# Kernel optimization log

Measured on AMD Instinct MI355X. Metric: run time of the kernel, lower is better.

The kernel has to match this reference:

```python
import jax, jax.numpy as jnp
import numpy as np

CAPACITY_FACTOR = 1.0


def setup_inputs() -> dict:
    key = jax.random.key(0)
    k1, k2, k3, k4 = jax.random.split(key, 4)
    B, T, D, E, F = 4, 2048, 2048, 8, 8192
    hidden_states = jax.random.normal(k1, (B, T, D), dtype=jnp.float32)
    w_gate = jax.random.normal(k2, (D, E), dtype=jnp.float32) * 0.02
    w1 = jax.random.normal(k3, (E, D, F), dtype=jnp.float32) * 0.02
    w2 = jax.random.normal(k4, (E, F, D), dtype=jnp.float32) * 0.02
    return {"hidden_states": hidden_states, "w_gate": w_gate, "w1": w1, "w2": w2}


def _top1_gate(x, w_gate):
    # x: [S, D]; deepspeed top1gating (no noise, no rts, drop_tokens=True)
    S, E = x.shape[0], w_gate.shape[1]
    capacity = int(CAPACITY_FACTOR * S / E)
    logits = x @ w_gate                      # [S, E]
    gates = jax.nn.softmax(logits, axis=-1)  # [S, E]
    idx1 = jnp.argmax(gates, axis=-1)        # [S]
    mask1 = jax.nn.one_hot(idx1, E, dtype=gates.dtype)          # [S, E]
    locations1 = jnp.cumsum(mask1, axis=0) - mask1              # position within expert
    mask1 = mask1 * (locations1 < capacity)                     # drop over-capacity tokens
    locations1_s = jnp.sum(locations1 * mask1, axis=1).astype(jnp.int32)  # [S]
    gates_masked = gates * mask1                                # [S, E]
    loc_oh = jax.nn.one_hot(locations1_s, capacity, dtype=gates.dtype) * jnp.sum(mask1, axis=1, keepdims=True)
    combine_weights = jnp.einsum('se,sc->sec', gates_masked, loc_oh)      # [S, E, C]
    dispatch_mask = (combine_weights > 0).astype(gates.dtype)             # [S, E, C]
    return combine_weights, dispatch_mask


def reference(hidden_states, w_gate, w1, w2):
    B, T, D = hidden_states.shape
    x = hidden_states.reshape(-1, D)                     # [S, D]
    combine_weights, dispatch_mask = _top1_gate(x, w_gate)
    # dense dispatch: [S,E,C] x [S,D] -> [E,C,D]
    dispatched = jnp.einsum('sec,sm->ecm', dispatch_mask, x)
    # per-expert FFN (GELU MLP), batched over experts
    h = jax.nn.gelu(jnp.einsum('ecd,edf->ecf', dispatched, w1))
    expert_out = jnp.einsum('ecf,efd->ecd', h, w2)       # [E, C, D]
    # dense combine: [S,E,C] x [E,C,D] -> [S,D]
    combined = jnp.einsum('sec,ecm->sm', combine_weights, expert_out)
    return combined.reshape(B, T, D)
```

## Files before the change

### kernel.cpp

```cpp
#include <hip/hip_runtime.h>

using u16 = unsigned short;
typedef __attribute__((ext_vector_type(4))) float f32x4;
typedef __attribute__((ext_vector_type(8))) short bf16x8;
typedef unsigned short u16x8 __attribute__((ext_vector_type(8)));

static constexpr int S_TOK = 8192;
static constexpr int NE    = 8;
static constexpr int CAP   = 1024;
static constexpr int DDIM  = 2048;
static constexpr int FDIM  = 8192;

#define S_WAIT_ALL() asm volatile("s_waitcnt vmcnt(0) lgkmcnt(0)" ::: "memory")
#define S_BAR()                                  \
  do {                                           \
    __builtin_amdgcn_sched_barrier(0);           \
    __builtin_amdgcn_s_barrier();                \
    __builtin_amdgcn_sched_barrier(0);           \
  } while (0)

__device__ __forceinline__ u16 f2bf(float f) {
  union { float fv; unsigned uv; } v; v.fv = f;
  unsigned r = v.uv + 0x7fffu + ((v.uv >> 16) & 1u);
  return (u16)(r >> 16);
}

__device__ __forceinline__ float gelu_tanh(float x) {
  float u = 0.7978845608028654f * (x + 0.044715f * x * x * x);
  float t = 1.0f - 2.0f / (__expf(2.0f * u) + 1.0f);
  return 0.5f * x * (1.0f + t);
}

__device__ __forceinline__ void gl_lds16(const void* g, void* l) {
  __builtin_amdgcn_global_load_lds(
      (const __attribute__((address_space(1))) unsigned int*)g,
      (__attribute__((address_space(3))) unsigned int*)l, 16, 0, 0);
}

__global__ __launch_bounds__(256) void fill_zero_kernel(float4* __restrict__ p, int n4) {
  int i = blockIdx.x * 256 + threadIdx.x;
  int stride = gridDim.x * 256;
  float4 z = {0.f, 0.f, 0.f, 0.f};
  for (; i < n4; i += stride) p[i] = z;
}

__global__ __launch_bounds__(256) void gating_kernel(
    const float* __restrict__ x, const float* __restrict__ wg,
    int* __restrict__ tok_expert, float* __restrict__ tok_gate) {
  int s = blockIdx.x * 4 + (threadIdx.x >> 6);
  int lane = threadIdx.x & 63;
  const float4* xv = (const float4*)(x + (size_t)s * DDIM + lane * 32);
  float acc[8];
#pragma unroll
  for (int e = 0; e < 8; ++e) acc[e] = 0.f;
#pragma unroll
  for (int j = 0; j < 8; ++j) {
    float4 xx = xv[j];
#pragma unroll
    for (int c = 0; c < 4; ++c) {
      int i = lane * 32 + j * 4 + c;
      const float4* wrow = (const float4*)(wg + (size_t)i * 8);
      float4 w0 = wrow[0], w1 = wrow[1];
      float xe = (c == 0) ? xx.x : (c == 1) ? xx.y : (c == 2) ? xx.z : xx.w;
      acc[0] += xe * w0.x; acc[1] += xe * w0.y; acc[2] += xe * w0.z; acc[3] += xe * w0.w;
      acc[4] += xe * w1.x; acc[5] += xe * w1.y; acc[6] += xe * w1.z; acc[7] += xe * w1.w;
    }
  }
#pragma unroll
  for (int off = 32; off > 0; off >>= 1)
#pragma unroll
    for (int e = 0; e < 8; ++e) acc[e] += __shfl_xor(acc[e], off, 64);
  if (lane == 0) {
    float m = acc[0]; int ai = 0;
#pragma unroll
    for (int e = 1; e < 8; ++e) if (acc[e] > m) { m = acc[e]; ai = e; }
    float sum = 0.f;
#pragma unroll
    for (int e = 0; e < 8; ++e) sum += expf(acc[e] - m);
    tok_expert[s] = ai;
    tok_gate[s] = 1.0f / sum;
  }
}

__global__ void init_slots(int* tok_of_slot, float* gate_of_slot) {
  int i = blockIdx.x * 256 + threadIdx.x;
  tok_of_slot[i] = -1;
  gate_of_slot[i] = 0.f;
}

__global__ __launch_bounds__(1024) void scan_kernel(
    const int* __restrict__ tok_expert, const float* __restrict__ tok_gate,
    int* __restrict__ tok_of_slot, float* __restrict__ gate_of_slot) {
  __shared__ int cnt[1024][8];
  int t = threadIdx.x;
  int e8[8];
  int local[8];
#pragma unroll
  for (int e = 0; e < 8; ++e) local[e] = 0;
#pragma unroll
  for (int j = 0; j < 8; ++j) {
    int e = tok_expert[t * 8 + j];
    e8[j] = e;
    local[e]++;
  }
#pragma unroll
  for (int e = 0; e < 8; ++e) cnt[t][e] = local[e];
  __syncthreads();
  for (int off = 1; off < 1024; off <<= 1) {
    int v[8];
    bool has = (t >= off);
    if (has) {
#pragma unroll
      for (int e = 0; e < 8; ++e) v[e] = cnt[t - off][e];
    }
    __syncthreads();
    if (has) {
#pragma unroll
      for (int e = 0; e < 8; ++e) cnt[t][e] += v[e];
    }
    __syncthreads();
  }
  int base[8];
#pragma unroll
  for (int e = 0; e < 8; ++e) base[e] = (t == 0) ? 0 : cnt[t - 1][e];
#pragma unroll
  for (int j = 0; j < 8; ++j) {
    int s = t * 8 + j;
    int e = e8[j];
    int p = base[e]++;
    if (p < CAP) {
      tok_of_slot[e * CAP + p] = s;
      gate_of_slot[e * CAP + p] = tok_gate[s];
    }
  }
}

__global__ __launch_bounds__(256) void scatter_kernel(
    const int* __restrict__ tok_of_slot, const float* __restrict__ x,
    u16* __restrict__ Xd) {
  int slot = blockIdx.x;
  int s = tok_of_slot[slot];
  int t = threadIdx.x;
  u16x8 v;
  if (s >= 0) {
    const float4* xr = (const float4*)(x + (size_t)s * DDIM + t * 8);
    float4 a = xr[0], b = xr[1];
    v[0] = f2bf(a.x); v[1] = f2bf(a.y); v[2] = f2bf(a.z); v[3] = f2bf(a.w);
    v[4] = f2bf(b.x); v[5] = f2bf(b.y); v[6] = f2bf(b.z); v[7] = f2bf(b.w);
  } else {
#pragma unroll
    for (int j = 0; j < 8; ++j) v[j] = 0;
  }
  *(u16x8*)(Xd + (size_t)slot * DDIM + t * 8) = v;
}

template <int KDIM, int NDIM, int EPI, int NEXP>
__global__ __launch_bounds__(512, 2) void moe_gemm(
    const u16* __restrict__ A, const float* __restrict__ Bf,
    u16* __restrict__ Hout, float* __restrict__ Fout,
    const int* __restrict__ tok_of_slot, const float* __restrict__ gate_of_slot,
    int e_base) {
  constexpr int MDIM = 1024;
  constexpr int BM = 256, BN = 256, BK = 64;
  constexpr int MT = MDIM / BM;
  constexpr int NK = KDIM / BK;
  constexpr int ASZ = BM * BK;
  constexpr int BSZ = BN * BK;
  constexpr int BUFSZ = ASZ + BSZ;
  __shared__ u16 lds[2 * BUFSZ];

  const int t = threadIdx.x;
  const int lane = t & 63, wave = t >> 6;
  const int wr = wave >> 2, wc = wave & 3;

  int id = blockIdx.x;
  int ez = id & (NEXP - 1);
  int w = id / NEXP;
  int mt = w & (MT - 1);
  int nt = w / MT;
  int m0 = mt * BM, n0 = nt * BN;
  int e = e_base + ez;

  const u16* Ae = A + (size_t)ez * MDIM * KDIM;
  const float* Be = Bf + (size_t)ez * (size_t)KDIM * NDIM;

  const u16* aSrc[4];
  int ldsOffA[4];
#pragma unroll
  for (int p = 0; p < 4; ++p) {
    int c = t + p * 512;
    int row = c >> 3;
    int j = (c & 7) ^ (row & 7);
    aSrc[p] = Ae + (size_t)(m0 + row) * KDIM + j * 8;
    ldsOffA[p] = c * 8;
  }

  const int bq = (t & 63) * 4;
  const int boct = t >> 6;
  const float* bP = Be + (size_t)(boct * 8) * NDIM + n0 + bq;
  int bWOff[4];
#pragma unroll
  for (int c = 0; c < 4; ++c) {
    int row = bq + c;
    bWOff[c] = ASZ + row * 64 + (boct ^ (row & 7)) * 8;
  }

  const int aBase = (wr * 128 + (lane & 15)) * 64;
  const int bBase = ASZ + (wc * 64 + (lane & 15)) * 64;
  const int swz = (lane & 7) << 4;
  const int cK0 = ((((lane >> 4) * 16)) ^ swz) >> 1;
  const int cK1 = ((64 + (lane >> 4) * 16) ^ swz) >> 1;

  f32x4 acc[8][4];
#pragma unroll
  for (int m = 0; m < 8; ++m)
#pragma unroll
    for (int n = 0; n < 4; ++n) acc[m][n] = f32x4{0.f, 0.f, 0.f, 0.f};

  f32x4 bv4[8];

#pragma unroll
  for (int p = 0; p < 4; ++p) gl_lds16(aSrc[p], &lds[ldsOffA[p]]);
#pragma unroll
  for (int j = 0; j < 8; ++j) bv4[j] = *(const f32x4*)(bP + (size_t)j * NDIM);
#pragma unroll
  for (int c = 0; c < 4; ++c) {
    u16x8 o;
#pragma unroll
    for (int j = 0; j < 8; ++j) o[j] = f2bf(bv4[j][c]);
    *(u16x8*)(&lds[bWOff[c]]) = o;
  }
  S_WAIT_ALL();
  S_BAR();

  for (int kt = 0; kt < NK; ++kt) {
    const u16* sb = &lds[(kt & 1) * BUFSZ];
    u16* nb = &lds[((kt + 1) & 1) * BUFSZ];
    const bool pre = (kt + 1 < NK);
    if (pre) {
      const int ko = (kt + 1) * BK;
#pragma unroll
      for (int p = 0; p < 4; ++p) gl_lds16(aSrc[p] + ko, nb + ldsOffA[p]);
#pragma unroll
      for (int j = 0; j < 8; ++j)
        bv4[j] = *(const f32x4*)(bP + (size_t)(ko + j) * NDIM);
    }

#pragma unroll
    for (int kk = 0; kk < 2; ++kk) {
      const int ck = kk ? cK1 : cK0;
      bf16x8 af[8], bv[4];
#pragma unroll
      for (int m = 0; m < 8; ++m)
        af[m] = *(const bf16x8*)(sb + aBase + m * 1024 + ck);
#pragma unroll
      for (int n = 0; n < 4; ++n)
        bv[n] = *(const bf16x8*)(sb + bBase + n * 1024 + ck);
      __builtin_amdgcn_s_setprio(1);
#pragma unroll
      for (int m = 0; m < 8; ++m)
#pragma unroll
        for (int n = 0; n < 4; ++n)
          acc[m][n] = __builtin_amdgcn_mfma_f32_16x16x32_bf16(af[m], bv[n], acc[m][n], 0, 0, 0);
      __builtin_amdgcn_s_setprio(0);
    }

    if (pre) {
#pragma unroll
      for (int c = 0; c < 4; ++c) {
        u16x8 o;
#pragma unroll
        for (int j = 0; j < 8; ++j) o[j] = f2bf(bv4[j][c]);
        *(u16x8*)(nb + bWOff[c]) = o;
      }
    }
    S_WAIT_ALL();
    S_BAR();
  }

  if (EPI == 0) {
    u16* Hrow = Hout + (size_t)ez * MDIM * NDIM;
#pragma unroll
    for (int m = 0; m < 8; ++m) {
#pragma unroll
      for (int r = 0; r < 4; ++r) {
        int row = m0 + wr * 128 + m * 16 + (lane >> 4) * 4 + r;
#pragma unroll
        for (int n = 0; n < 4; ++n) {
          int col = n0 + wc * 64 + n * 16 + (lane & 15);
          Hrow[(size_t)row * NDIM + col] = f2bf(gelu_tanh(acc[m][n][r]));
        }
      }
    }
  } else {
#pragma unroll
    for (int m = 0; m < 8; ++m) {
#pragma unroll
      for (int r = 0; r < 4; ++r) {
        int slot_in_e = m0 + wr * 128 + m * 16 + (lane >> 4) * 4 + r;
        int gslot = e * CAP + slot_in_e;
        int s = tok_of_slot[gslot];
        if (s >= 0) {
          float g = gate_of_slot[gslot];
#pragma unroll
          for (int n = 0; n < 4; ++n) {
            int col = n0 + wc * 64 + n * 16 + (lane & 15);
            Fout[(size_t)s * NDIM + col] = g * acc[m][n][r];
          }
        }
      }
    }
  }
}

extern "C" void kernel_launch(void* const* d_in, const int* in_sizes, int n_in,
                              void* d_out, int out_size, void* d_ws, size_t ws_size,
                              hipStream_t stream) {
  (void)in_sizes; (void)n_in;
  const float* x  = (const float*)d_in[0];
  const float* wg = (const float*)d_in[1];
  const float* w1 = (const float*)d_in[2];
  const float* w2 = (const float*)d_in[3];
  float* out = (float*)d_out;

  char* ws = (char*)d_ws;
  size_t off = 0;
  auto alloc = [&](size_t b) {
    off = (off + 255) & ~(size_t)255;
    char* p = ws + off;
    off += b;
    return p;
  };
  int*   tok_expert   = (int*)alloc((size_t)S_TOK * 4);
  float* tok_gate     = (float*)alloc((size_t)S_TOK * 4);
  int*   tok_of_slot  = (int*)alloc((size_t)NE * CAP * 4);
  float* gate_of_slot = (float*)alloc((size_t)NE * CAP * 4);
  u16*   Xd           = (u16*)alloc((size_t)NE * CAP * DDIM * 2);
  size_t off_common = off;

  const size_t H_big = (size_t)NE * CAP * FDIM * 2;
  const size_t H_sm  = (size_t)CAP * FDIM * 2;
  bool big = ws_size >= off_common + H_big + 1024;

  fill_zero_kernel<<<2048, 256, 0, stream>>>((float4*)out, out_size / 4);
  gating_kernel<<<S_TOK / 4, 256, 0, stream>>>(x, wg, tok_expert, tok_gate);
  init_slots<<<(NE * CAP) / 256, 256, 0, stream>>>(tok_of_slot, gate_of_slot);
  scan_kernel<<<1, 1024, 0, stream>>>(tok_expert, tok_gate, tok_of_slot, gate_of_slot);
  scatter_kernel<<<NE * CAP, 256, 0, stream>>>(tok_of_slot, x, Xd);

  if (big) {
    u16* H = (u16*)alloc(H_big);
    moe_gemm<DDIM, FDIM, 0, NE><<<dim3(NE * 4 * (FDIM / 256)), 512, 0, stream>>>(
        Xd, w1, H, nullptr, tok_of_slot, gate_of_slot, 0);
    moe_gemm<FDIM, DDIM, 1, NE><<<dim3(NE * 4 * (DDIM / 256)), 512, 0, stream>>>(
        H, w2, nullptr, out, tok_of_slot, gate_of_slot, 0);
  } else {
    u16* H = (u16*)alloc(H_sm);
    for (int e = 0; e < NE; ++e) {
      moe_gemm<DDIM, FDIM, 0, 1><<<dim3(4 * (FDIM / 256)), 512, 0, stream>>>(
          Xd + (size_t)e * CAP * DDIM, w1 + (size_t)e * DDIM * FDIM, H, nullptr,
          tok_of_slot, gate_of_slot, e);
      moe_gemm<FDIM, DDIM, 1, 1><<<dim3(4 * (DDIM / 256)), 512, 0, stream>>>(
          H, w2 + (size_t)e * FDIM * DDIM, nullptr, out,
          tok_of_slot, gate_of_slot, e);
    }
  }
}
```

Before: 762.3 us.

## Split GEMM k-loop into four interleaved phases with fine-grained waitcnt

Restructures the main GEMM loop into four MFMA phases, each preceded by a partial LDS fragment load. The global A-tile prefetches are spread across the phases, and barriers separate them. The single wait-all is replaced by targeted vmcnt/lgkmcnt waits, so the B fp32 loads can finish while other copies are still in flight. The aim is to overlap LDS reads, global copies and MFMA more finely, in a ping-pong style, at the cost of more barriers per iteration.

```diff
diff --git a/kernel.cpp b/kernel.cpp
--- a/kernel.cpp
+++ b/kernel.cpp
@@ -11,7 +11,10 @@
 static constexpr int DDIM  = 2048;
 static constexpr int FDIM  = 8192;
 
-#define S_WAIT_ALL() asm volatile("s_waitcnt vmcnt(0) lgkmcnt(0)" ::: "memory")
+#define S_VMCNT(n) do { asm volatile("s_waitcnt vmcnt(" #n ")" ::: "memory"); \
+                        __builtin_amdgcn_sched_barrier(0); } while (0)
+#define LGKM0()    do { asm volatile("s_waitcnt lgkmcnt(0)" ::: "memory");    \
+                        __builtin_amdgcn_sched_barrier(0); } while (0)
 #define S_BAR()                                  \
   do {                                           \
     __builtin_amdgcn_sched_barrier(0);           \
@@ -220,9 +223,10 @@
   f32x4 bv4[8];
 
 #pragma unroll
+  for (int j = 0; j < 8; ++j) bv4[j] = *(const f32x4*)(bP + (size_t)j * NDIM);
+#pragma unroll
   for (int p = 0; p < 4; ++p) gl_lds16(aSrc[p], &lds[ldsOffA[p]]);
-#pragma unroll
-  for (int j = 0; j < 8; ++j) bv4[j] = *(const f32x4*)(bP + (size_t)j * NDIM);
+  S_VMCNT(4);
 #pragma unroll
   for (int c = 0; c < 4; ++c) {
     u16x8 o;
@@ -230,42 +234,84 @@
     for (int j = 0; j < 8; ++j) o[j] = f2bf(bv4[j][c]);
     *(u16x8*)(&lds[bWOff[c]]) = o;
   }
-  S_WAIT_ALL();
+  S_VMCNT(0);
+  LGKM0();
   S_BAR();
 
   for (int kt = 0; kt < NK; ++kt) {
     const u16* sb = &lds[(kt & 1) * BUFSZ];
     u16* nb = &lds[((kt + 1) & 1) * BUFSZ];
     const bool pre = (kt + 1 < NK);
+    const int ko = (kt + 1) * BK;
+
+    bf16x8 afA[4], afB[4], bv0[4], bv1[4];
+
+#pragma unroll
+    for (int mi = 0; mi < 4; ++mi)
+      afA[mi] = *(const bf16x8*)(sb + aBase + mi * 1024 + cK0);
+#pragma unroll
+    for (int n = 0; n < 4; ++n)
+      bv0[n] = *(const bf16x8*)(sb + bBase + n * 1024 + cK0);
     if (pre) {
-      const int ko = (kt + 1) * BK;
-#pragma unroll
-      for (int p = 0; p < 4; ++p) gl_lds16(aSrc[p] + ko, nb + ldsOffA[p]);
 #pragma unroll
       for (int j = 0; j < 8; ++j)
         bv4[j] = *(const f32x4*)(bP + (size_t)(ko + j) * NDIM);
     }
-
-#pragma unroll
-    for (int kk = 0; kk < 2; ++kk) {
-      const int ck = kk ? cK1 : cK0;
-      bf16x8 af[8], bv[4];
-#pragma unroll
-      for (int m = 0; m < 8; ++m)
-        af[m] = *(const bf16x8*)(sb + aBase + m * 1024 + ck);
+    S_BAR();
+    LGKM0();
+    __builtin_amdgcn_s_setprio(1);
+#pragma unroll
+    for (int mi = 0; mi < 4; ++mi)
 #pragma unroll
       for (int n = 0; n < 4; ++n)
-        bv[n] = *(const bf16x8*)(sb + bBase + n * 1024 + ck);
-      __builtin_amdgcn_s_setprio(1);
-#pragma unroll
-      for (int m = 0; m < 8; ++m)
-#pragma unroll
-        for (int n = 0; n < 4; ++n)
-          acc[m][n] = __builtin_amdgcn_mfma_f32_16x16x32_bf16(af[m], bv[n], acc[m][n], 0, 0, 0);
-      __builtin_amdgcn_s_setprio(0);
-    }
-
+        acc[mi][n] = __builtin_amdgcn_mfma_f32_16x16x32_bf16(afA[mi], bv0[n], acc[mi][n], 0, 0, 0);
+    __builtin_amdgcn_s_setprio(0);
+    S_BAR();
+
+#pragma unroll
+    for (int mi = 0; mi < 4; ++mi)
+      afB[mi] = *(const bf16x8*)(sb + aBase + (4 + mi) * 1024 + cK0);
     if (pre) {
+      gl_lds16(aSrc[0] + ko, nb + ldsOffA[0]);
+      gl_lds16(aSrc[1] + ko, nb + ldsOffA[1]);
+    }
+    S_BAR();
+    LGKM0();
+    __builtin_amdgcn_s_setprio(1);
+#pragma unroll
+    for (int mi = 0; mi < 4; ++mi)
+#pragma unroll
+      for (int n = 0; n < 4; ++n)
+        acc[4 + mi][n] = __builtin_amdgcn_mfma_f32_16x16x32_bf16(afB[mi], bv0[n], acc[4 + mi][n], 0, 0, 0);
+    __builtin_amdgcn_s_setprio(0);
+    S_BAR();
+
+#pragma unroll
+    for (int mi = 0; mi < 4; ++mi)
+      afA[mi] = *(const bf16x8*)(sb + aBase + mi * 1024 + cK1);
+#pragma unroll
+    for (int n = 0; n < 4; ++n)
+      bv1[n] = *(const bf16x8*)(sb + bBase + n * 1024 + cK1);
+    if (pre) {
+      gl_lds16(aSrc[2] + ko, nb + ldsOffA[2]);
+      gl_lds16(aSrc[3] + ko, nb + ldsOffA[3]);
+    }
+    S_BAR();
+    LGKM0();
+    __builtin_amdgcn_s_setprio(1);
+#pragma unroll
+    for (int mi = 0; mi < 4; ++mi)
+#pragma unroll
+      for (int n = 0; n < 4; ++n)
+        acc[mi][n] = __builtin_amdgcn_mfma_f32_16x16x32_bf16(afA[mi], bv1[n], acc[mi][n], 0, 0, 0);
+    __builtin_amdgcn_s_setprio(0);
+    S_BAR();
+
+#pragma unroll
+    for (int mi = 0; mi < 4; ++mi)
+      afB[mi] = *(const bf16x8*)(sb + aBase + (4 + mi) * 1024 + cK1);
+    if (pre) {
+      S_VMCNT(4);
 #pragma unroll
       for (int c = 0; c < 4; ++c) {
         u16x8 o;
@@ -274,7 +320,16 @@
         *(u16x8*)(nb + bWOff[c]) = o;
       }
     }
-    S_WAIT_ALL();
+    LGKM0();
+    S_BAR();
+    __builtin_amdgcn_s_setprio(1);
+#pragma unroll
+    for (int mi = 0; mi < 4; ++mi)
+#pragma unroll
+      for (int n = 0; n < 4; ++n)
+        acc[4 + mi][n] = __builtin_amdgcn_mfma_f32_16x16x32_bf16(afB[mi], bv1[n], acc[4 + mi][n], 0, 0, 0);
+    __builtin_amdgcn_s_setprio(0);
+    if (pre) S_VMCNT(0);
     S_BAR();
   }
 
```

After: 860.4 us. 1.13x slower.
